# Kernel tuning notes

Measured on AMD Instinct MI355X. Metric: run time of the kernel, lower is better.

The kernel has to match this reference:

```python
import jax, jax.numpy as jnp
import numpy as np

DIM = 96; QK = 96; MLP = 192; HEADS = 6; NTOK = 8; GS = 128; KS = 5
B, D, H, W = 2, 8, 64, 64


def _ln(x, g, b, eps=1e-5):
    m = x.mean(-1, keepdims=True)
    v = x.var(-1, keepdims=True)
    return (x - m) / jnp.sqrt(v + eps) * g + b


def _l2(x, eps=1e-12):
    n = jnp.linalg.norm(x, axis=-1, keepdims=True)
    return x / jnp.maximum(n, eps)


def setup_inputs() -> dict:
    key = jax.random.key(0)
    ks = jax.random.split(key, 16)
    p = lambda i, shape: jax.random.normal(ks[i], shape, jnp.float32) * 0.02
    return dict(
        x=jax.random.normal(ks[0], (B, DIM, D, H, W), jnp.float32),
        means=jax.random.normal(ks[1], (NTOK, DIM), jnp.float32),
        ln1_g=jnp.ones((DIM,), jnp.float32), ln1_b=jnp.zeros((DIM,), jnp.float32),
        Wkg=p(2, (DIM, QK)), Wvg=p(3, (DIM, DIM)),
        Wq=p(4, (DIM, QK)), Wk=p(5, (DIM, QK)), Wv=p(6, (DIM, DIM)), Wproj=p(7, (DIM, DIM)),
        Wconv=p(8, (DIM, DIM)),
        ln2_g=jnp.ones((DIM,), jnp.float32), ln2_b=jnp.zeros((DIM,), jnp.float32),
        W1=p(9, (DIM, MLP)), b1=jnp.zeros((MLP,), jnp.float32),
        Wdw=p(10, (MLP, 1, KS, KS, KS)), bdw=jnp.zeros((MLP,), jnp.float32),
        W2=p(11, (MLP, DIM)), b2=jnp.zeros((DIM,), jnp.float32),
    )


def reference(x, means, ln1_g, ln1_b, Wkg, Wvg, Wq, Wk, Wv, Wproj, Wconv,
              ln2_g, ln2_b, W1, b1, Wdw, bdw, W2, b2):
    b, c, d, h, w = x.shape
    N = d * h * w
    xt = x.reshape(b, c, N).transpose(0, 2, 1)          # b n c
    residual = xt
    xn = _ln(xt, ln1_g, ln1_b)

    # IRCA (eval, initted=True): k/v from cluster means (buffer, detached)
    mns = jax.lax.stop_gradient(means)
    kg = (mns @ Wkg).reshape(NTOK, HEADS, QK // HEADS).transpose(1, 0, 2)  # h t dq
    vg = (mns @ Wvg).reshape(NTOK, HEADS, c // HEADS).transpose(1, 0, 2)   # h t dv

    # cluster assignment + sort (no_grad in torch)
    scores = _l2(jax.lax.stop_gradient(xn)) @ _l2(mns).T                   # b n t
    belong = jnp.argmax(scores, axis=-1)
    idx = jnp.argsort(belong, axis=-1)                                     # b n

    # IASA: project, gather by cluster-sorted index
    q = xn @ Wq; k = xn @ Wk; v = xn @ Wv
    take = lambda t: jnp.take_along_axis(t, idx[..., None], axis=1)
    qs, ks_, vs = take(q), take(k), take(v)

    gs = min(N, GS)
    ng = N // gs                      # N chosen divisible by gs -> pad_n = 0
    dq = QK // HEADS; dv = c // HEADS
    qb = qs.reshape(b, ng, gs, HEADS, dq).transpose(0, 1, 3, 2, 4)  # b ng h gs dq

    def windows(t, dh):
        # append reversed last group, then take overlapping 2*gs windows, stride gs
        tp = jnp.concatenate([t, t[:, N - gs:][:, ::-1]], axis=1)   # b (ng+1)*gs .
        blk = tp.reshape(b, ng + 1, gs, HEADS, dh)
        wnd = jnp.concatenate([blk[:, :-1], blk[:, 1:]], axis=2)    # b ng 2gs h dh
        return wnd.transpose(0, 1, 3, 2, 4)                         # b ng h 2gs dh

    kw = windows(ks_, dq)
    vw = windows(vs, dv)
    scale = float(1.0 / np.sqrt(dq))

    a1 = jax.nn.softmax(jnp.einsum('bghqd,bghkd->bghqk', qb, kw) * scale, axis=-1)
    out1 = jnp.einsum('bghqk,bghkd->bghqd', a1, vw)
    a2 = jax.nn.softmax(jnp.einsum('bghqd,htd->bghqt', qb, kg) * scale, axis=-1)
    out2 = jnp.einsum('bghqt,htd->bghqd', a2, vg)

    out = (out1 + out2).transpose(0, 1, 3, 2, 4).reshape(b, N, c)   # sorted order
    inv = jnp.argsort(idx, axis=-1)                                  # scatter back
    out = jnp.take_along_axis(out, inv[..., None], axis=1)
    out = out @ Wproj

    y = out @ Wconv                      # 1x1x1 conv3d == channel matmul
    xr = residual + y

    # PreNorm ConvFFN3D
    z = _ln(xr, ln2_g, ln2_b)
    z = jax.nn.gelu(z @ W1 + b1, approximate=False)
    zv = z.transpose(0, 2, 1).reshape(b, MLP, d, h, w)
    pad = (KS - 1) // 2
    dwo = jax.lax.conv_general_dilated(
        zv, Wdw, (1, 1, 1), [(pad, pad)] * 3,
        feature_group_count=MLP, dimension_numbers=('NCDHW', 'OIDHW', 'NCDHW'))
    dwo = jax.nn.gelu(dwo + bdw.reshape(1, MLP, 1, 1, 1), approximate=False)
    z = z + dwo.reshape(b, MLP, N).transpose(0, 2, 1)
    z = z @ W2 + b2

    return (z + xr).transpose(0, 2, 1).reshape(b, c, d, h, w)
```

## Files before the change

### kernel.cpp

```cpp
#include <hip/hip_runtime.h>
#include <math.h>

#define NB 2
#define NC 96
#define ND 8
#define NHH 64
#define NWW 64
#define NN 32768
#define NTOK 8
#define NHEADS 6
#define GSZ 128
#define NGRP 256
#define NMLP 192

typedef float4 f4;

__device__ __forceinline__ float gelu_f(float x) {
    return 0.5f * x * (1.0f + erff(x * 0.70710678118654752440f));
}

__global__ void __launch_bounds__(256) k_precompute(
    const float* __restrict__ means, const float* __restrict__ g1, const float* __restrict__ b1v,
    const float* __restrict__ Wkg, const float* __restrict__ Wvg,
    const float* __restrict__ Wproj, const float* __restrict__ Wconv,
    float* __restrict__ mnn, float* __restrict__ gdot, float* __restrict__ bdot,
    float* __restrict__ kg, float* __restrict__ vg, float* __restrict__ wpc) {
    int blk = blockIdx.x; int tid = threadIdx.x;
    if (blk == 0) {
        __shared__ float mlds[NTOK*NC];
        __shared__ float glds[NC], blds[NC];
        for (int i = tid; i < NTOK*NC; i += 256) mlds[i] = means[i];
        if (tid < NC) { glds[tid] = g1[tid]; blds[tid] = b1v[tid]; }
        __syncthreads();
        if (tid < NTOK) {
            float ss = 0.f;
            for (int c = 0; c < NC; ++c) { float v = mlds[tid*NC+c]; ss += v*v; }
            float inv = 1.0f / fmaxf(sqrtf(ss), 1e-12f);
            float gd = 0.f, bd = 0.f;
            for (int c = 0; c < NC; ++c) {
                float v = mlds[tid*NC+c] * inv;
                mnn[tid*NC+c] = v;
                gd += glds[c]*v; bd += blds[c]*v;
            }
            gdot[tid] = gd; bdot[tid] = bd;
        }
        for (int i = tid; i < NHEADS*NTOK*16; i += 256) {
            int h = i / (NTOK*16); int r = i % (NTOK*16); int t = r / 16; int e = r % 16;
            float sk = 0.f, sv = 0.f;
            for (int c = 0; c < NC; ++c) {
                float mv = mlds[t*NC+c];
                sk += mv * Wkg[c*NC + h*16+e];
                sv += mv * Wvg[c*NC + h*16+e];
            }
            kg[i] = sk; vg[i] = sv;
        }
    } else {
        int r0 = (blk-1)*24;
        __shared__ float wcv[NC][NC];
        __shared__ float wpl[24][NC];
        for (int i = tid; i < NC*NC; i += 256) wcv[i/NC][i%NC] = Wconv[i];
        for (int i = tid; i < 24*NC; i += 256) wpl[i/NC][i%NC] = Wproj[(r0 + i/NC)*NC + i%NC];
        __syncthreads();
        for (int o = tid; o < 24*NC; o += 256) {
            int r = o / NC, c = o % NC;
            float s = 0.f;
            for (int k = 0; k < NC; ++k) s += wpl[r][k]*wcv[k][c];
            wpc[(r0+r)*NC + c] = s;
        }
    }
}

__global__ void __launch_bounds__(256) k_ln1(
    const float* __restrict__ x, const float* __restrict__ g1, const float* __restrict__ b1v,
    const float* __restrict__ mnn, const float* __restrict__ gdot, const float* __restrict__ bdot,
    float* __restrict__ xn, int* __restrict__ belong) {
    __shared__ __align__(16) float xt[NC][68];
    __shared__ float meanl[64], rstdl[64];
    __shared__ float gl[NC], bl[NC], gdl[NTOK], bdl[NTOK];
    int b = blockIdx.y; int n0 = blockIdx.x * 64;
    int tid = threadIdx.x;
    if (tid < NC) { gl[tid] = g1[tid]; bl[tid] = b1v[tid]; }
    if (tid >= NC && tid < NC+NTOK) { gdl[tid-NC] = gdot[tid-NC]; bdl[tid-NC] = bdot[tid-NC]; }
    for (int i = tid; i < NC*64; i += 256) {
        int c = i >> 6, n = i & 63;
        xt[c][n] = x[((size_t)b*NC + c)*NN + n0 + n];
    }
    __syncthreads();
    int lane = tid & 63, w = tid >> 6;
    float ga = gl[lane];
    float gb = (lane < 32) ? gl[64+lane] : 0.f;
    float ma[NTOK], mb[NTOK];
#pragma unroll
    for (int t = 0; t < NTOK; ++t) {
        ma[t] = mnn[t*NC + lane];
        mb[t] = (lane < 32) ? mnn[t*NC + 64 + lane] : 0.f;
    }
    for (int tk = 0; tk < 16; ++tk) {
        int tok = w*16 + tk;
        float a  = xt[lane][tok];
        float bb = (lane < 32) ? xt[64+lane][tok] : 0.f;
        float red[10];
        red[0] = a + bb;
        red[1] = a*a + bb*bb;
        float ag = a*ga, bg = bb*gb;
#pragma unroll
        for (int t = 0; t < NTOK; ++t) red[2+t] = ag*ma[t] + bg*mb[t];
#pragma unroll
        for (int off = 32; off > 0; off >>= 1) {
#pragma unroll
            for (int r = 0; r < 10; ++r) red[r] += __shfl_xor(red[r], off);
        }
        if (lane == 0) {
            float mean = red[0] * (1.0f/NC);
            float var  = red[1] * (1.0f/NC) - mean*mean;
            float rstd = rsqrtf(var + 1e-5f);
            meanl[tok] = mean; rstdl[tok] = rstd;
            int best = 0; float bestv = -1e30f;
#pragma unroll
            for (int t = 0; t < NTOK; ++t) {
                float sc = rstd*(red[2+t] - mean*gdl[t]) + bdl[t];
                if (sc > bestv) { bestv = sc; best = t; }
            }
            belong[b*NN + n0 + tok] = best;
        }
    }
    __syncthreads();
    for (int i = tid; i < 64*NC; i += 256) {
        int n = i / NC, c = i % NC;
        float v = (xt[c][n] - meanl[n]) * rstdl[n] * gl[c] + bl[c];
        xn[((size_t)b*NN + n0 + n)*NC + c] = v;
    }
}

__global__ void __launch_bounds__(256) k_hist(const int* __restrict__ belong, int* __restrict__ hist) {
    int b = blockIdx.y, ch = blockIdx.x, tid = threadIdx.x;
    __shared__ int wc[4][NTOK];
    int myt = belong[b*NN + ch*256 + tid];
    int w = tid >> 6, lane = tid & 63;
#pragma unroll
    for (int t = 0; t < NTOK; ++t) {
        unsigned long long m = __ballot(myt == t);
        if (lane == 0) wc[w][t] = __popcll(m);
    }
    __syncthreads();
    if (tid < NTOK) hist[(b*128 + ch)*NTOK + tid] = wc[0][tid]+wc[1][tid]+wc[2][tid]+wc[3][tid];
}

__global__ void __launch_bounds__(256) k_scan(const int* __restrict__ hist, int* __restrict__ base) {
    int b = blockIdx.x, tid = threadIdx.x;
    __shared__ int A[NTOK][128], Bf[NTOK][128], orig[NTOK][128];
    __shared__ int cb[NTOK];
    for (int i = tid; i < NTOK*128; i += 256) {
        int t = i >> 7, ch = i & 127;
        int v = hist[(b*128 + ch)*NTOK + t];
        A[t][ch] = v; orig[t][ch] = v;
    }
    __syncthreads();
    for (int d = 1; d < 128; d <<= 1) {
        for (int i = tid; i < NTOK*128; i += 256) {
            int t = i >> 7, ch = i & 127;
            Bf[t][ch] = A[t][ch] + ((ch >= d) ? A[t][ch-d] : 0);
        }
        __syncthreads();
        for (int i = tid; i < NTOK*128; i += 256) {
            int t = i >> 7, ch = i & 127;
            A[t][ch] = Bf[t][ch];
        }
        __syncthreads();
    }
    if (tid == 0) {
        int run = 0;
        for (int t = 0; t < NTOK; ++t) { cb[t] = run; run += A[t][127]; }
    }
    __syncthreads();
    for (int i = tid; i < NTOK*128; i += 256) {
        int t = i >> 7, ch = i & 127;
        base[(b*128 + ch)*NTOK + t] = cb[t] + A[t][ch] - orig[t][ch];
    }
}

__global__ void __launch_bounds__(256) k_scatteridx(
    const int* __restrict__ belong, const int* __restrict__ base,
    int* __restrict__ idx, int* __restrict__ inv) {
    int b = blockIdx.y, ch = blockIdx.x, tid = threadIdx.x;
    __shared__ int wc[4][NTOK];
    __shared__ int woff[4][NTOK];
    int n = ch*256 + tid;
    int myt = belong[b*NN + n];
    int w = tid >> 6, lane = tid & 63;
    unsigned long long mymask = 0;
#pragma unroll
    for (int t = 0; t < NTOK; ++t) {
        unsigned long long m = __ballot(myt == t);
        if (myt == t) mymask = m;
        if (lane == 0) wc[w][t] = __popcll(m);
    }
    __syncthreads();
    if (tid < 32) {
        int w2 = tid >> 3, t = tid & 7;
        int s = 0;
        for (int ww = 0; ww < w2; ++ww) s += wc[ww][t];
        woff[w2][t] = s;
    }
    __syncthreads();
    int rank = __popcll(mymask & ((1ull << lane) - 1ull));
    int p = base[(b*128+ch)*NTOK + myt] + woff[w][myt] + rank;
    idx[b*NN + p] = n;
    inv[b*NN + n] = p;
}

__global__ void __launch_bounds__(256) k_qkv(
    const float* __restrict__ xn, const int* __restrict__ idx,
    const float* __restrict__ Wq, const float* __restrict__ Wk, const float* __restrict__ Wv,
    float* __restrict__ qs, float* __restrict__ ks, float* __restrict__ vs) {
    __shared__ __align__(16) float xnT[NC][132];
    __shared__ __align__(16) float wch[32][NC];
    __shared__ int idxl[128];
    int b = blockIdx.y; int p0 = blockIdx.x * 128; int tid = threadIdx.x;
    if (tid < 128) idxl[tid] = idx[b*NN + p0 + tid];
    __syncthreads();
    for (int i = tid; i < 128*NC; i += 256) {
        int p = i / NC, c = i % NC;
        xnT[c][p] = xn[((size_t)b*NN + idxl[p])*NC + c];
    }
    int cx = tid & 15, ny = tid >> 4;
    const float* Ws[3] = {Wq, Wk, Wv};
    float* Os[3] = {qs, ks, vs};
    for (int m = 0; m < 3; ++m) {
        float acc[8][6];
#pragma unroll
        for (int i = 0; i < 8; ++i)
#pragma unroll
            for (int j = 0; j < 6; ++j) acc[i][j] = 0.f;
        const float* W = Ws[m];
        for (int kc = 0; kc < NC; kc += 32) {
            __syncthreads();
            for (int i = tid; i < 32*NC; i += 256) {
                int kk = i / NC, c = i % NC;
                wch[kk][c] = W[(kc+kk)*NC + c];
            }
            __syncthreads();
            for (int kk = 0; kk < 32; ++kk) {
                f4 a0 = *(const f4*)&xnT[kc+kk][ny*8];
                f4 a1 = *(const f4*)&xnT[kc+kk][ny*8+4];
                float a[8] = {a0.x,a0.y,a0.z,a0.w,a1.x,a1.y,a1.z,a1.w};
                float2 w0 = *(const float2*)&wch[kk][cx*6];
                float2 w1 = *(const float2*)&wch[kk][cx*6+2];
                float2 w2 = *(const float2*)&wch[kk][cx*6+4];
                float bb[6] = {w0.x,w0.y,w1.x,w1.y,w2.x,w2.y};
#pragma unroll
                for (int i = 0; i < 8; ++i)
#pragma unroll
                    for (int j = 0; j < 6; ++j) acc[i][j] += a[i]*bb[j];
            }
        }
        float* O = Os[m];
#pragma unroll
        for (int i = 0; i < 8; ++i) {
            size_t off = ((size_t)b*NN + p0 + ny*8 + i)*NC + cx*6;
            float2 s0 = {acc[i][0], acc[i][1]};
            float2 s1 = {acc[i][2], acc[i][3]};
            float2 s2 = {acc[i][4], acc[i][5]};
            *(float2*)&O[off]   = s0;
            *(float2*)&O[off+2] = s1;
            *(float2*)&O[off+4] = s2;
        }
    }
}

__global__ void __launch_bounds__(256) k_attn(
    const float* __restrict__ qs, const float* __restrict__ ks, const float* __restrict__ vs,
    const float* __restrict__ kg, const float* __restrict__ vg,
    float* __restrict__ attn) {
    __shared__ __align__(16) f4 kt[256][4];
    __shared__ __align__(16) f4 vt[256][4];
    __shared__ __align__(16) f4 kgs[NTOK][4];
    __shared__ __align__(16) f4 vgs[NTOK][4];
    int g = blockIdx.x, h = blockIdx.y, b = blockIdx.z;
    int tid = threadIdx.x;
    for (int i = tid; i < 1024; i += 256) {
        int r = i >> 2, c = i & 3;
        int src = g*GSZ + r;
        if (g == NGRP-1 && r >= GSZ) src = NN - 1 - (r - GSZ);
        size_t off = ((size_t)b*NN + src)*NC + h*16 + c*4;
        kt[r][c] = *(const f4*)&ks[off];
        vt[r][c] = *(const f4*)&vs[off];
    }
    if (tid < 32) {
        int t = tid >> 2, c = tid & 3;
        kgs[t][c] = *(const f4*)&kg[(h*NTOK + t)*16 + c*4];
        vgs[t][c] = *(const f4*)&vg[(h*NTOK + t)*16 + c*4];
    }
    int wv = tid >> 6, lane = tid & 63;
    int row = wv*32 + (lane & 31);
    int half = lane >> 5;
    float qv[16];
    {
        const f4* qp = (const f4*)&qs[((size_t)b*NN + g*GSZ + row)*NC + h*16];
#pragma unroll
        for (int i = 0; i < 4; ++i) {
            f4 t = qp[i];
            qv[i*4+0]=t.x*0.25f; qv[i*4+1]=t.y*0.25f; qv[i*4+2]=t.z*0.25f; qv[i*4+3]=t.w*0.25f;
        }
    }
    __syncthreads();
    float m = -1e30f, l = 0.f;
    float acc[16];
#pragma unroll
    for (int e = 0; e < 16; ++e) acc[e] = 0.f;
    int k0 = half * GSZ;
    for (int c8 = 0; c8 < 16; ++c8) {
        float s[8];
#pragma unroll
        for (int j = 0; j < 8; ++j) {
            const f4* kp = &kt[k0 + c8*8 + j][0];
            f4 ka = kp[0], kb = kp[1], kc = kp[2], kd = kp[3];
            s[j] = qv[0]*ka.x + qv[1]*ka.y + qv[2]*ka.z + qv[3]*ka.w
                 + qv[4]*kb.x + qv[5]*kb.y + qv[6]*kb.z + qv[7]*kb.w
                 + qv[8]*kc.x + qv[9]*kc.y + qv[10]*kc.z + qv[11]*kc.w
                 + qv[12]*kd.x + qv[13]*kd.y + qv[14]*kd.z + qv[15]*kd.w;
        }
        float cm = fmaxf(fmaxf(fmaxf(s[0],s[1]), fmaxf(s[2],s[3])),
                         fmaxf(fmaxf(s[4],s[5]), fmaxf(s[6],s[7])));
        float nm = fmaxf(m, cm);
        float corr = __expf(m - nm);
        m = nm;
        l *= corr;
#pragma unroll
        for (int e = 0; e < 16; ++e) acc[e] *= corr;
#pragma unroll
        for (int j = 0; j < 8; ++j) {
            float p = __expf(s[j] - m);
            l += p;
            const f4* vp = &vt[k0 + c8*8 + j][0];
            f4 va = vp[0], vb = vp[1], vc = vp[2], vd = vp[3];
            acc[0] += p*va.x; acc[1] += p*va.y; acc[2] += p*va.z; acc[3] += p*va.w;
            acc[4] += p*vb.x; acc[5] += p*vb.y; acc[6] += p*vb.z; acc[7] += p*vb.w;
            acc[8] += p*vc.x; acc[9] += p*vc.y; acc[10] += p*vc.z; acc[11] += p*vc.w;
            acc[12] += p*vd.x; acc[13] += p*vd.y; acc[14] += p*vd.z; acc[15] += p*vd.w;
        }
    }
    float m2 = -1e30f, l2 = 0.f;
    float a2[16];
#pragma unroll
    for (int e = 0; e < 16; ++e) a2[e] = 0.f;
#pragma unroll
    for (int t = 0; t < NTOK; ++t) {
        f4 ka = kgs[t][0], kb = kgs[t][1], kc = kgs[t][2], kd = kgs[t][3];
        float s = qv[0]*ka.x + qv[1]*ka.y + qv[2]*ka.z + qv[3]*ka.w
                + qv[4]*kb.x + qv[5]*kb.y + qv[6]*kb.z + qv[7]*kb.w
                + qv[8]*kc.x + qv[9]*kc.y + qv[10]*kc.z + qv[11]*kc.w
                + qv[12]*kd.x + qv[13]*kd.y + qv[14]*kd.z + qv[15]*kd.w;
        float nm2 = fmaxf(m2, s);
        float corr = __expf(m2 - nm2);
        m2 = nm2;
        l2 *= corr;
        float p = __expf(s - m2);
        l2 += p;
        f4 va = vgs[t][0], vb = vgs[t][1], vc = vgs[t][2], vd = vgs[t][3];
#pragma unroll
        for (int e = 0; e < 16; ++e) a2[e] *= corr;
        a2[0] += p*va.x; a2[1] += p*va.y; a2[2] += p*va.z; a2[3] += p*va.w;
        a2[4] += p*vb.x; a2[5] += p*vb.y; a2[6] += p*vb.z; a2[7] += p*vb.w;
        a2[8] += p*vc.x; a2[9] += p*vc.y; a2[10] += p*vc.z; a2[11] += p*vc.w;
        a2[12] += p*vd.x; a2[13] += p*vd.y; a2[14] += p*vd.z; a2[15] += p*vd.w;
    }
    float inv2 = 1.f / l2;
    float om = __shfl_xor(m, 32);
    float ol = __shfl_xor(l, 32);
    float mw = fmaxf(m, om);
    float es = __expf(m - mw), eo = __expf(om - mw);
    float lw = l*es + ol*eo;
    float invw = 1.f / lw;
    float o[16];
#pragma unroll
    for (int e = 0; e < 16; ++e) {
        float oa = __shfl_xor(acc[e], 32);
        o[e] = (acc[e]*es + oa*eo)*invw + a2[e]*inv2;
    }
    if (half == 0) {
        f4* op = (f4*)&attn[((size_t)b*NN + g*GSZ + row)*NC + h*16];
#pragma unroll
        for (int i = 0; i < 4; ++i) {
            f4 t = {o[i*4+0], o[i*4+1], o[i*4+2], o[i*4+3]};
            op[i] = t;
        }
    }
}

__global__ void __launch_bounds__(256) k_scatproj(
    const float* __restrict__ attn, const int* __restrict__ inv,
    const float* __restrict__ wpc, const float* __restrict__ x,
    float* __restrict__ xrt) {
    __shared__ __align__(16) float attT[NC][68];
    __shared__ __align__(16) float wch[32][NC];
    __shared__ int invl[64];
    int b = blockIdx.y; int n0 = blockIdx.x * 64; int tid = threadIdx.x;
    if (tid < 64) invl[tid] = inv[b*NN + n0 + tid];
    __syncthreads();
    for (int i = tid; i < 64*NC; i += 256) {
        int n = i / NC, c = i % NC;
        attT[c][n] = attn[((size_t)b*NN + invl[n])*NC + c];
    }
    int nx = tid & 15, cy = tid >> 4;
    float acc[4][6];
#pragma unroll
    for (int i = 0; i < 4; ++i)
#pragma unroll
        for (int j = 0; j < 6; ++j) acc[i][j] = 0.f;
    for (int kc = 0; kc < NC; kc += 32) {
        __syncthreads();
        for (int i = tid; i < 32*NC; i += 256) {
            int kk = i / NC, c = i % NC;
            wch[kk][c] = wpc[(kc+kk)*NC + c];
        }
        __syncthreads();
        for (int kk = 0; kk < 32; ++kk) {
            f4 a0 = *(const f4*)&attT[kc+kk][nx*4];
            float a[4] = {a0.x,a0.y,a0.z,a0.w};
            float2 w0 = *(const float2*)&wch[kk][cy*6];
            float2 w1 = *(const float2*)&wch[kk][cy*6+2];
            float2 w2 = *(const float2*)&wch[kk][cy*6+4];
            float bb[6] = {w0.x,w0.y,w1.x,w1.y,w2.x,w2.y};
#pragma unroll
            for (int i = 0; i < 4; ++i)
#pragma unroll
                for (int j = 0; j < 6; ++j) acc[i][j] += a[i]*bb[j];
        }
    }
#pragma unroll
    for (int j = 0; j < 6; ++j) {
        int c = cy*6 + j;
        size_t off = ((size_t)b*NC + c)*NN + n0 + nx*4;
        f4 xv = *(const f4*)&x[off];
        f4 o = {acc[0][j]+xv.x, acc[1][j]+xv.y, acc[2][j]+xv.z, acc[3][j]+xv.w};
        *(f4*)&xrt[off] = o;
    }
}

__global__ void __launch_bounds__(256) k_mlp1(
    const float* __restrict__ xrt, const float* __restrict__ g2, const float* __restrict__ b2v,
    const float* __restrict__ W1, const float* __restrict__ b1m,
    float* __restrict__ z1t) {
    __shared__ __align__(16) float xt[NC][68];
    __shared__ __align__(16) float wch[32][NMLP];
    __shared__ float meanl[64], rstdl[64];
    __shared__ float gl[NC], bl[NC];
    int b = blockIdx.y; int n0 = blockIdx.x*64; int tid = threadIdx.x;
    if (tid < NC) { gl[tid] = g2[tid]; bl[tid] = b2v[tid]; }
    for (int i = tid; i < NC*64; i += 256) {
        int c = i >> 6, n = i & 63;
        xt[c][n] = xrt[((size_t)b*NC + c)*NN + n0 + n];
    }
    __syncthreads();
    int lane = tid & 63, w = tid >> 6;
    for (int tk = 0; tk < 16; ++tk) {
        int tok = w*16 + tk;
        float a  = xt[lane][tok];
        float bb = (lane < 32) ? xt[64+lane][tok] : 0.f;
        float s = a + bb, sq = a*a + bb*bb;
#pragma unroll
        for (int off = 32; off > 0; off >>= 1) {
            s  += __shfl_xor(s, off);
            sq += __shfl_xor(sq, off);
        }
        if (lane == 0) {
            float mean = s * (1.0f/NC);
            float var  = sq * (1.0f/NC) - mean*mean;
            meanl[tok] = mean; rstdl[tok] = rsqrtf(var + 1e-5f);
        }
    }
    __syncthreads();
    for (int i = tid; i < NC*64; i += 256) {
        int c = i >> 6, n = i & 63;
        xt[c][n] = (xt[c][n]-meanl[n])*rstdl[n]*gl[c]+bl[c];
    }
    int nx = tid & 15, my = tid >> 4;
    float acc[4][12];
#pragma unroll
    for (int i = 0; i < 4; ++i)
#pragma unroll
        for (int j = 0; j < 12; ++j) acc[i][j] = 0.f;
    for (int kc = 0; kc < NC; kc += 32) {
        __syncthreads();
        for (int i = tid; i < 32*NMLP; i += 256) {
            int kk = i / NMLP, c = i % NMLP;
            wch[kk][c] = W1[(kc+kk)*NMLP + c];
        }
        __syncthreads();
        for (int kk = 0; kk < 32; ++kk) {
            f4 a0 = *(const f4*)&xt[kc+kk][nx*4];
            float a[4] = {a0.x,a0.y,a0.z,a0.w};
            f4 w0 = *(const f4*)&wch[kk][my*12];
            f4 w1 = *(const f4*)&wch[kk][my*12+4];
            f4 w2 = *(const f4*)&wch[kk][my*12+8];
            float bb[12] = {w0.x,w0.y,w0.z,w0.w,w1.x,w1.y,w1.z,w1.w,w2.x,w2.y,w2.z,w2.w};
#pragma unroll
            for (int i = 0; i < 4; ++i)
#pragma unroll
                for (int j = 0; j < 12; ++j) acc[i][j] += a[i]*bb[j];
        }
    }
#pragma unroll
    for (int j = 0; j < 12; ++j) {
        int mm = my*12 + j;
        float bias = b1m[mm];
        size_t off = ((size_t)b*NMLP + mm)*NN + n0 + nx*4;
        f4 o = { gelu_f(acc[0][j]+bias), gelu_f(acc[1][j]+bias),
                 gelu_f(acc[2][j]+bias), gelu_f(acc[3][j]+bias) };
        *(f4*)&z1t[off] = o;
    }
}

__global__ void __launch_bounds__(256) k_dwconv(
    const float* __restrict__ z1t, const float* __restrict__ Wdw, const float* __restrict__ bdw,
    float* __restrict__ z2t) {
    __shared__ __align__(16) float tin[ND][20][72];
    __shared__ float wl[128];
    int ht = blockIdx.x, mch = blockIdx.y, b = blockIdx.z;
    int h0 = ht*16; int tid = threadIdx.x;
    if (tid < 125) wl[tid] = Wdw[mch*125 + tid];
    const float* src = &z1t[((size_t)b*NMLP + mch)*NN];
    for (int i = tid; i < ND*20*68; i += 256) {
        int dd = i / (20*68); int r = i % (20*68); int hh = r / 68; int ww = r % 68;
        int gh = h0 + hh - 2, gw = ww - 2;
        float v = 0.f;
        if ((unsigned)gh < 64u && (unsigned)gw < 64u) v = src[dd*4096 + gh*64 + gw];
        tin[dd][hh][ww] = v;
    }
    __syncthreads();
    int rowid = tid >> 1; int od = rowid >> 4; int ohl = rowid & 15; int wb = (tid & 1)*32;
    float acc[32];
#pragma unroll
    for (int o = 0; o < 32; ++o) acc[o] = 0.f;
    for (int kd = 0; kd < 5; ++kd) {
        int id = od + kd - 2;
        if ((unsigned)id >= (unsigned)ND) continue;
#pragma unroll
        for (int kh = 0; kh < 5; ++kh) {
            const float* rp = &tin[id][ohl+kh][wb];
            float seg[36];
#pragma unroll
            for (int i = 0; i < 9; ++i) *(f4*)&seg[i*4] = *(const f4*)&rp[i*4];
#pragma unroll
            for (int kw = 0; kw < 5; ++kw) {
                float wt = wl[kd*25 + kh*5 + kw];
#pragma unroll
                for (int o = 0; o < 32; ++o) acc[o] += seg[o+kw]*wt;
            }
        }
    }
    float bias = bdw[mch];
    float* dst = &z2t[((size_t)b*NMLP + mch)*NN + od*4096 + (size_t)(h0+ohl)*64 + wb];
    const float* ctr = &tin[od][ohl+2][wb+2];
#pragma unroll
    for (int o4 = 0; o4 < 32; o4 += 4) {
        f4 ov = { ctr[o4+0] + gelu_f(acc[o4+0]+bias),
                  ctr[o4+1] + gelu_f(acc[o4+1]+bias),
                  ctr[o4+2] + gelu_f(acc[o4+2]+bias),
                  ctr[o4+3] + gelu_f(acc[o4+3]+bias) };
        *(f4*)&dst[o4] = ov;
    }
}

__global__ void __launch_bounds__(256) k_final(
    const float* __restrict__ z2t, const float* __restrict__ W2, const float* __restrict__ b2m,
    const float* __restrict__ xrt, float* __restrict__ out) {
    __shared__ __align__(16) float zch[32][132];
    __shared__ __align__(16) float wch[32][NC];
    int b = blockIdx.y; int n0 = blockIdx.x*128; int tid = threadIdx.x;
    int nx = tid & 15, cy = tid >> 4;
    float acc[8][6];
#pragma unroll
    for (int i = 0; i < 8; ++i)
#pragma unroll
        for (int j = 0; j < 6; ++j) acc[i][j] = 0.f;
    for (int kc = 0; kc < NMLP; kc += 32) {
        __syncthreads();
        for (int i = tid; i < 32*128; i += 256) {
            int kk = i >> 7, n = i & 127;
            zch[kk][n] = z2t[((size_t)b*NMLP + kc + kk)*NN + n0 + n];
        }
        for (int i = tid; i < 32*NC; i += 256) {
            int kk = i / NC, c = i % NC;
            wch[kk][c] = W2[(kc+kk)*NC + c];
        }
        __syncthreads();
        for (int kk = 0; kk < 32; ++kk) {
            f4 a0 = *(const f4*)&zch[kk][nx*8];
            f4 a1 = *(const f4*)&zch[kk][nx*8+4];
            float a[8] = {a0.x,a0.y,a0.z,a0.w,a1.x,a1.y,a1.z,a1.w};
            float2 w0 = *(const float2*)&wch[kk][cy*6];
            float2 w1 = *(const float2*)&wch[kk][cy*6+2];
            float2 w2 = *(const float2*)&wch[kk][cy*6+4];
            float bb[6] = {w0.x,w0.y,w1.x,w1.y,w2.x,w2.y};
#pragma unroll
            for (int i = 0; i < 8; ++i)
#pragma unroll
                for (int j = 0; j < 6; ++j) acc[i][j] += a[i]*bb[j];
        }
    }
#pragma unroll
    for (int j = 0; j < 6; ++j) {
        int c = cy*6 + j;
        float bias = b2m[c];
        size_t off = ((size_t)b*NC + c)*NN + n0 + nx*8;
        f4 x0 = *(const f4*)&xrt[off];
        f4 x1 = *(const f4*)&xrt[off+4];
        f4 o0 = {acc[0][j]+bias+x0.x, acc[1][j]+bias+x0.y, acc[2][j]+bias+x0.z, acc[3][j]+bias+x0.w};
        f4 o1 = {acc[4][j]+bias+x1.x, acc[5][j]+bias+x1.y, acc[6][j]+bias+x1.z, acc[7][j]+bias+x1.w};
        *(f4*)&out[off]   = o0;
        *(f4*)&out[off+4] = o1;
    }
}

extern "C" void kernel_launch(void* const* d_in, const int* in_sizes, int n_in,
                              void* d_out, int out_size, void* d_ws, size_t ws_size,
                              hipStream_t stream) {
    (void)in_sizes; (void)n_in; (void)out_size; (void)ws_size;
    const float* x     = (const float*)d_in[0];
    const float* means = (const float*)d_in[1];
    const float* ln1_g = (const float*)d_in[2];
    const float* ln1_b = (const float*)d_in[3];
    const float* Wkg   = (const float*)d_in[4];
    const float* Wvg   = (const float*)d_in[5];
    const float* Wq    = (const float*)d_in[6];
    const float* Wk    = (const float*)d_in[7];
    const float* Wv    = (const float*)d_in[8];
    const float* Wproj = (const float*)d_in[9];
    const float* Wconv = (const float*)d_in[10];
    const float* ln2_g = (const float*)d_in[11];
    const float* ln2_b = (const float*)d_in[12];
    const float* W1    = (const float*)d_in[13];
    const float* b1    = (const float*)d_in[14];
    const float* Wdw   = (const float*)d_in[15];
    const float* bdw   = (const float*)d_in[16];
    const float* W2    = (const float*)d_in[17];
    const float* b2    = (const float*)d_in[18];
    float* out = (float*)d_out;

    float* ws = (float*)d_ws;
    const size_t SZ = (size_t)NB*NN*NC;
    float* xn   = ws;
    float* qs   = ws + SZ;
    float* ks   = ws + 2*SZ;
    float* vs   = ws + 3*SZ;
    float* attn = ws + 4*SZ;
    float* xrt  = ws;
    float* z1t  = ws + SZ;
    float* z2t  = ws + 3*SZ;
    float* faux = ws + 5*SZ;
    float* mnn  = faux;
    float* gdot = faux + 768;
    float* bdot = faux + 776;
    float* kg   = faux + 784;
    float* vg   = faux + 1552;
    float* wpc  = faux + 2320;
    int* iaux   = (int*)(faux + 11536);
    int* belong = iaux;
    int* idx    = iaux + NB*NN;
    int* inv    = iaux + 2*NB*NN;
    int* hist   = iaux + 3*NB*NN;
    int* baseb  = hist + NB*128*NTOK;

    k_precompute<<<dim3(5), dim3(256), 0, stream>>>(
        means, ln1_g, ln1_b, Wkg, Wvg, Wproj, Wconv, mnn, gdot, bdot, kg, vg, wpc);
    k_ln1<<<dim3(NN/64, NB), dim3(256), 0, stream>>>(
        x, ln1_g, ln1_b, mnn, gdot, bdot, xn, belong);
    k_hist<<<dim3(NN/256, NB), dim3(256), 0, stream>>>(belong, hist);
    k_scan<<<dim3(NB), dim3(256), 0, stream>>>(hist, baseb);
    k_scatteridx<<<dim3(NN/256, NB), dim3(256), 0, stream>>>(belong, baseb, idx, inv);
    k_qkv<<<dim3(NN/128, NB), dim3(256), 0, stream>>>(xn, idx, Wq, Wk, Wv, qs, ks, vs);
    k_attn<<<dim3(NGRP, NHEADS, NB), dim3(256), 0, stream>>>(qs, ks, vs, kg, vg, attn);
    k_scatproj<<<dim3(NN/64, NB), dim3(256), 0, stream>>>(attn, inv, wpc, x, xrt);
    k_mlp1<<<dim3(NN/64, NB), dim3(256), 0, stream>>>(xrt, ln2_g, ln2_b, W1, b1, z1t);
    k_dwconv<<<dim3(4, NMLP, NB), dim3(256), 0, stream>>>(z1t, Wdw, bdw, z2t);
    k_final<<<dim3(NN/128, NB), dim3(256), 0, stream>>>(z2t, W2, b2, xrt, out);
}
```

Measured before the change: 639.2 us.

## Process two query rows per thread in group attention to reuse K/V loads

```diff
diff --git a/kernel.cpp b/kernel.cpp
--- a/kernel.cpp
+++ b/kernel.cpp
@@ -292,94 +292,128 @@
         vgs[t][c] = *(const f4*)&vg[(h*NTOK + t)*16 + c*4];
     }
     int wv = tid >> 6, lane = tid & 63;
-    int row = wv*32 + (lane & 31);
-    int half = lane >> 5;
-    float qv[16];
+    int pr = lane & 15;
+    int qt = lane >> 4;
+    int r0 = wv*32 + pr*2;
+    float qv0[16], qv1[16];
     {
-        const f4* qp = (const f4*)&qs[((size_t)b*NN + g*GSZ + row)*NC + h*16];
+        const f4* qp0 = (const f4*)&qs[((size_t)b*NN + g*GSZ + r0)*NC + h*16];
+        const f4* qp1 = (const f4*)&qs[((size_t)b*NN + g*GSZ + r0 + 1)*NC + h*16];
 #pragma unroll
         for (int i = 0; i < 4; ++i) {
-            f4 t = qp[i];
-            qv[i*4+0]=t.x*0.25f; qv[i*4+1]=t.y*0.25f; qv[i*4+2]=t.z*0.25f; qv[i*4+3]=t.w*0.25f;
-        }
-    }
-    __syncthreads();
-    float m = -1e30f, l = 0.f;
-    float acc[16];
-#pragma unroll
-    for (int e = 0; e < 16; ++e) acc[e] = 0.f;
-    int k0 = half * GSZ;
-    for (int c8 = 0; c8 < 16; ++c8) {
-        float s[8];
+            f4 t0 = qp0[i], t1 = qp1[i];
+            qv0[i*4+0]=t0.x*0.25f; qv0[i*4+1]=t0.y*0.25f; qv0[i*4+2]=t0.z*0.25f; qv0[i*4+3]=t0.w*0.25f;
+            qv1[i*4+0]=t1.x*0.25f; qv1[i*4+1]=t1.y*0.25f; qv1[i*4+2]=t1.z*0.25f; qv1[i*4+3]=t1.w*0.25f;
+        }
+    }
+    __syncthreads();
+    float m0 = -1e30f, l0 = 0.f, m1 = -1e30f, l1 = 0.f;
+    float acc0[16], acc1[16];
+#pragma unroll
+    for (int e = 0; e < 16; ++e) { acc0[e] = 0.f; acc1[e] = 0.f; }
+    int k0 = qt * 64;
+    for (int c8 = 0; c8 < 8; ++c8) {
+        float s0[8], s1[8];
 #pragma unroll
         for (int j = 0; j < 8; ++j) {
             const f4* kp = &kt[k0 + c8*8 + j][0];
             f4 ka = kp[0], kb = kp[1], kc = kp[2], kd = kp[3];
-            s[j] = qv[0]*ka.x + qv[1]*ka.y + qv[2]*ka.z + qv[3]*ka.w
-                 + qv[4]*kb.x + qv[5]*kb.y + qv[6]*kb.z + qv[7]*kb.w
-                 + qv[8]*kc.x + qv[9]*kc.y + qv[10]*kc.z + qv[11]*kc.w
-                 + qv[12]*kd.x + qv[13]*kd.y + qv[14]*kd.z + qv[15]*kd.w;
-        }
-        float cm = fmaxf(fmaxf(fmaxf(s[0],s[1]), fmaxf(s[2],s[3])),
-                         fmaxf(fmaxf(s[4],s[5]), fmaxf(s[6],s[7])));
-        float nm = fmaxf(m, cm);
-        float corr = __expf(m - nm);
-        m = nm;
-        l *= corr;
-#pragma unroll
-        for (int e = 0; e < 16; ++e) acc[e] *= corr;
+            s0[j] = qv0[0]*ka.x + qv0[1]*ka.y + qv0[2]*ka.z + qv0[3]*ka.w
+                  + qv0[4]*kb.x + qv0[5]*kb.y + qv0[6]*kb.z + qv0[7]*kb.w
+                  + qv0[8]*kc.x + qv0[9]*kc.y + qv0[10]*kc.z + qv0[11]*kc.w
+                  + qv0[12]*kd.x + qv0[13]*kd.y + qv0[14]*kd.z + qv0[15]*kd.w;
+            s1[j] = qv1[0]*ka.x + qv1[1]*ka.y + qv1[2]*ka.z + qv1[3]*ka.w
+                  + qv1[4]*kb.x + qv1[5]*kb.y + qv1[6]*kb.z + qv1[7]*kb.w
+                  + qv1[8]*kc.x + qv1[9]*kc.y + qv1[10]*kc.z + qv1[11]*kc.w
+                  + qv1[12]*kd.x + qv1[13]*kd.y + qv1[14]*kd.z + qv1[15]*kd.w;
+        }
+        float cm0 = fmaxf(fmaxf(fmaxf(s0[0],s0[1]), fmaxf(s0[2],s0[3])),
+                          fmaxf(fmaxf(s0[4],s0[5]), fmaxf(s0[6],s0[7])));
+        float cm1 = fmaxf(fmaxf(fmaxf(s1[0],s1[1]), fmaxf(s1[2],s1[3])),
+                          fmaxf(fmaxf(s1[4],s1[5]), fmaxf(s1[6],s1[7])));
+        float nm0 = fmaxf(m0, cm0), nm1 = fmaxf(m1, cm1);
+        float corr0 = __expf(m0 - nm0), corr1 = __expf(m1 - nm1);
+        m0 = nm0; m1 = nm1;
+        l0 *= corr0; l1 *= corr1;
+#pragma unroll
+        for (int e = 0; e < 16; ++e) { acc0[e] *= corr0; acc1[e] *= corr1; }
 #pragma unroll
         for (int j = 0; j < 8; ++j) {
-            float p = __expf(s[j] - m);
-            l += p;
+            float p0 = __expf(s0[j] - m0);
+            float p1 = __expf(s1[j] - m1);
+            l0 += p0; l1 += p1;
             const f4* vp = &vt[k0 + c8*8 + j][0];
             f4 va = vp[0], vb = vp[1], vc = vp[2], vd = vp[3];
-            acc[0] += p*va.x; acc[1] += p*va.y; acc[2] += p*va.z; acc[3] += p*va.w;
-            acc[4] += p*vb.x; acc[5] += p*vb.y; acc[6] += p*vb.z; acc[7] += p*vb.w;
-            acc[8] += p*vc.x; acc[9] += p*vc.y; acc[10] += p*vc.z; acc[11] += p*vc.w;
-            acc[12] += p*vd.x; acc[13] += p*vd.y; acc[14] += p*vd.z; acc[15] += p*vd.w;
-        }
-    }
-    float m2 = -1e30f, l2 = 0.f;
-    float a2[16];
-#pragma unroll
-    for (int e = 0; e < 16; ++e) a2[e] = 0.f;
-#pragma unroll
-    for (int t = 0; t < NTOK; ++t) {
-        f4 ka = kgs[t][0], kb = kgs[t][1], kc = kgs[t][2], kd = kgs[t][3];
-        float s = qv[0]*ka.x + qv[1]*ka.y + qv[2]*ka.z + qv[3]*ka.w
-                + qv[4]*kb.x + qv[5]*kb.y + qv[6]*kb.z + qv[7]*kb.w
-                + qv[8]*kc.x + qv[9]*kc.y + qv[10]*kc.z + qv[11]*kc.w
-                + qv[12]*kd.x + qv[13]*kd.y + qv[14]*kd.z + qv[15]*kd.w;
-        float nm2 = fmaxf(m2, s);
-        float corr = __expf(m2 - nm2);
-        m2 = nm2;
-        l2 *= corr;
-        float p = __expf(s - m2);
-        l2 += p;
-        f4 va = vgs[t][0], vb = vgs[t][1], vc = vgs[t][2], vd = vgs[t][3];
-#pragma unroll
-        for (int e = 0; e < 16; ++e) a2[e] *= corr;
-        a2[0] += p*va.x; a2[1] += p*va.y; a2[2] += p*va.z; a2[3] += p*va.w;
-        a2[4] += p*vb.x; a2[5] += p*vb.y; a2[6] += p*vb.z; a2[7] += p*vb.w;
-        a2[8] += p*vc.x; a2[9] += p*vc.y; a2[10] += p*vc.z; a2[11] += p*vc.w;
-        a2[12] += p*vd.x; a2[13] += p*vd.y; a2[14] += p*vd.z; a2[15] += p*vd.w;
-    }
-    float inv2 = 1.f / l2;
-    float om = __shfl_xor(m, 32);
-    float ol = __shfl_xor(l, 32);
-    float mw = fmaxf(m, om);
-    float es = __expf(m - mw), eo = __expf(om - mw);
-    float lw = l*es + ol*eo;
-    float invw = 1.f / lw;
-    float o[16];
+            acc0[0] += p0*va.x; acc0[1] += p0*va.y; acc0[2] += p0*va.z; acc0[3] += p0*va.w;
+            acc0[4] += p0*vb.x; acc0[5] += p0*vb.y; acc0[6] += p0*vb.z; acc0[7] += p0*vb.w;
+            acc0[8] += p0*vc.x; acc0[9] += p0*vc.y; acc0[10] += p0*vc.z; acc0[11] += p0*vc.w;
+            acc0[12] += p0*vd.x; acc0[13] += p0*vd.y; acc0[14] += p0*vd.z; acc0[15] += p0*vd.w;
+            acc1[0] += p1*va.x; acc1[1] += p1*va.y; acc1[2] += p1*va.z; acc1[3] += p1*va.w;
+            acc1[4] += p1*vb.x; acc1[5] += p1*vb.y; acc1[6] += p1*vb.z; acc1[7] += p1*vb.w;
+            acc1[8] += p1*vc.x; acc1[9] += p1*vc.y; acc1[10] += p1*vc.z; acc1[11] += p1*vc.w;
+            acc1[12] += p1*vd.x; acc1[13] += p1*vd.y; acc1[14] += p1*vd.z; acc1[15] += p1*vd.w;
+        }
+    }
+#pragma unroll
+    for (int off = 16; off <= 32; off <<= 1) {
+        float om = __shfl_xor(m0, off), ol = __shfl_xor(l0, off);
+        float mw = fmaxf(m0, om);
+        float e0 = __expf(m0 - mw), e1 = __expf(om - mw);
+        l0 = l0*e0 + ol*e1; m0 = mw;
+#pragma unroll
+        for (int e = 0; e < 16; ++e) {
+            float oa = __shfl_xor(acc0[e], off);
+            acc0[e] = acc0[e]*e0 + oa*e1;
+        }
+        om = __shfl_xor(m1, off); ol = __shfl_xor(l1, off);
+        mw = fmaxf(m1, om);
+        e0 = __expf(m1 - mw); e1 = __expf(om - mw);
+        l1 = l1*e0 + ol*e1; m1 = mw;
+#pragma unroll
+        for (int e = 0; e < 16; ++e) {
+            float oa = __shfl_xor(acc1[e], off);
+            acc1[e] = acc1[e]*e0 + oa*e1;
+        }
+    }
+    float qvs[16], accs[16];
 #pragma unroll
     for (int e = 0; e < 16; ++e) {
-        float oa = __shfl_xor(acc[e], 32);
-        o[e] = (acc[e]*es + oa*eo)*invw + a2[e]*inv2;
-    }
-    if (half == 0) {
-        f4* op = (f4*)&attn[((size_t)b*NN + g*GSZ + row)*NC + h*16];
+        qvs[e]  = (qt == 1) ? qv1[e]  : qv0[e];
+        accs[e] = (qt == 1) ? acc1[e] : acc0[e];
+    }
+    float ls = (qt == 1) ? l1 : l0;
+    if (qt < 2) {
+        float m2 = -1e30f, l2 = 0.f;
+        float a2[16];
+#pragma unroll
+        for (int e = 0; e < 16; ++e) a2[e] = 0.f;
+#pragma unroll
+        for (int t = 0; t < NTOK; ++t) {
+            f4 ka = kgs[t][0], kb = kgs[t][1], kc = kgs[t][2], kd = kgs[t][3];
+            float s = qvs[0]*ka.x + qvs[1]*ka.y + qvs[2]*ka.z + qvs[3]*ka.w
+                    + qvs[4]*kb.x + qvs[5]*kb.y + qvs[6]*kb.z + qvs[7]*kb.w
+                    + qvs[8]*kc.x + qvs[9]*kc.y + qvs[10]*kc.z + qvs[11]*kc.w
+                    + qvs[12]*kd.x + qvs[13]*kd.y + qvs[14]*kd.z + qvs[15]*kd.w;
+            float nm2 = fmaxf(m2, s);
+            float corr = __expf(m2 - nm2);
+            m2 = nm2;
+            l2 *= corr;
+            float p = __expf(s - m2);
+            l2 += p;
+            f4 va = vgs[t][0], vb = vgs[t][1], vc = vgs[t][2], vd = vgs[t][3];
+#pragma unroll
+            for (int e = 0; e < 16; ++e) a2[e] *= corr;
+            a2[0] += p*va.x; a2[1] += p*va.y; a2[2] += p*va.z; a2[3] += p*va.w;
+            a2[4] += p*vb.x; a2[5] += p*vb.y; a2[6] += p*vb.z; a2[7] += p*vb.w;
+            a2[8] += p*vc.x; a2[9] += p*vc.y; a2[10] += p*vc.z; a2[11] += p*vc.w;
+            a2[12] += p*vd.x; a2[13] += p*vd.y; a2[14] += p*vd.z; a2[15] += p*vd.w;
+        }
+        float inv2 = 1.f / l2;
+        float invw = 1.f / ls;
+        float o[16];
+#pragma unroll
+        for (int e = 0; e < 16; ++e) o[e] = accs[e]*invw + a2[e]*inv2;
+        f4* op = (f4*)&attn[((size_t)b*NN + g*GSZ + r0 + qt)*NC + h*16];
 #pragma unroll
         for (int i = 0; i < 4; ++i) {
             f4 t = {o[i*4+0], o[i*4+1], o[i*4+2], o[i*4+3]};
```

Result: no change. 645.8 us (+1.0%).
